# Kernel tuning notes

Measured on AMD Instinct MI355X. Metric: run time of the kernel, lower is better.

The kernel has to match this reference:

```python
import jax, jax.numpy as jnp
import numpy as np

# SuperposedExpert: K parallel TT-factorized FFN paths + holographic routing.
# d_model=1024 factorized as [32,32]; d_ff=4096 as [64,64]; tt_ranks=[1,16,1] (r0/r2 squeezed).
K, D_MODEL, D_FF, RANK = 4, 1024, 4096, 16
IN1, IN2 = 32, 32          # factorize_for_tt(d_model)
F1, F2 = 64, 64            # factorize_for_tt(d_ff)
TEMP = 1.0                 # routing_temperature


def setup_inputs() -> dict:
    key = jax.random.key(0)
    ks = jax.random.split(key, 8)
    s = 0.05
    tokens = jax.random.normal(ks[0], (2048, D_MODEL), dtype=jnp.float32)
    # TT cores for ffn1: d_model -> d_ff  (input_dims [32,32], output_dims [64,64])
    ffn1_core1 = jax.random.normal(ks[1], (K, IN1, F1, RANK), dtype=jnp.float32) * s
    ffn1_core2 = jax.random.normal(ks[2], (K, RANK, IN2, F2), dtype=jnp.float32) * s
    # TT cores for ffn2: d_ff -> d_model (input_dims [64,64], output_dims [32,32])
    ffn2_core1 = jax.random.normal(ks[3], (K, F1, IN1, RANK), dtype=jnp.float32) * s
    ffn2_core2 = jax.random.normal(ks[4], (K, RANK, F2, IN2), dtype=jnp.float32) * s
    # Holographic routing params (hd_dim == d_model -> identity HD projection)
    pb = jax.random.normal(ks[5], (K, D_MODEL), dtype=jnp.float32)
    path_bases = pb / jnp.linalg.norm(pb, axis=-1, keepdims=True)  # orthogonal-ish init
    path_weights = jax.random.normal(ks[6], (K, D_MODEL), dtype=jnp.float32) * s
    return {
        'tokens': tokens,
        'ffn1_core1': ffn1_core1, 'ffn1_core2': ffn1_core2,
        'ffn2_core1': ffn2_core1, 'ffn2_core2': ffn2_core2,
        'path_bases': path_bases, 'path_weights': path_weights,
    }


def reference(tokens, ffn1_core1, ffn1_core2, ffn2_core1, ffn2_core2,
              path_bases, path_weights):
    N = tokens.shape[0]
    # ---- K superposed TT-FFN paths ----
    x3 = tokens.reshape(N, IN1, IN2)  # [n, a, b]
    # TT matmul 1: y[x,y] = sum_{a,b,r} G1[a,x,r] G2[r,b,y] x[a,b]
    h = jnp.einsum('nab,kaxr,krby->knxy', x3, ffn1_core1, ffn1_core2)
    h = jax.nn.gelu(h.reshape(K, N, D_FF))  # quantum_activation stand-in
    h3 = h.reshape(K, N, F1, F2)
    y = jnp.einsum('knab,kaxr,krby->knxy', h3, ffn2_core1, ffn2_core2)
    y = y.reshape(K, N, D_MODEL)  # per-path outputs
    # ---- Holographic HD routing (hd_dim == d_model: identity projection) ----
    logits = jnp.einsum('nd,kd->nk', tokens, path_bases) / TEMP
    gates = jax.nn.softmax(logits, axis=-1)  # [n, k]
    # Collapse superposition: per-path elementwise HD modulation + gated sum
    out = jnp.einsum('knd,kd,nk->nd', y, 1.0 + path_weights, gates)
    return out
```

## Files before the change

kernel.cpp:

```cpp
#include <hip/hip_runtime.h>
#include <stdint.h>

#define GAS __attribute__((address_space(1)))
#define LAS __attribute__((address_space(3)))

typedef __attribute__((ext_vector_type(8))) short short8;
typedef __attribute__((ext_vector_type(16))) float f32x16;

static constexpr int N_TOK = 2048;
static constexpr int DM    = 1024;
static constexpr int DF    = 4096;
static constexpr int KP    = 4;

__device__ inline unsigned short f2bf(float f) {
  union { float f; uint32_t u; } v; v.f = f;
  uint32_t u = v.u;
  u += 0x7FFFu + ((u >> 16) & 1u);
  return (unsigned short)(u >> 16);
}

__device__ inline uint32_t pk_bf(float lo, float hi) {
  union { float f; uint32_t u; } a, b; a.f = lo; b.f = hi;
  uint32_t ul = a.u + 0x7FFFu + ((a.u >> 16) & 1u);
  uint32_t uh = b.u + 0x7FFFu + ((b.u >> 16) & 1u);
  return (ul >> 16) | (uh & 0xFFFF0000u);
}

__device__ inline float gelu_gate(float v, float g) {
  float t0 = v * v;
  float u  = v * __builtin_fmaf(t0, -0.10294456f, -2.3022539f);
  float e  = __builtin_amdgcn_exp2f(u);
  float r  = __builtin_amdgcn_rcpf(1.0f + e);
  return v * g * r;
}

__device__ inline void gld16(const void* g, void* l) {
  __builtin_amdgcn_global_load_lds((const GAS void*)g, (LAS void*)l, 16, 0, 0);
}

__global__ __launch_bounds__(256) void setup_kernel(
    const float* __restrict__ tokens, const float* __restrict__ pb,
    const float* __restrict__ c11, const float* __restrict__ c12,
    const float* __restrict__ c21, const float* __restrict__ c22,
    float* __restrict__ gates, unsigned short* __restrict__ xb,
    unsigned short* __restrict__ w1t, unsigned short* __restrict__ w2t) {
  __shared__ __align__(16) float sh[2048];
  const int blk = blockIdx.x;
  const int t = threadIdx.x;
  if (blk < 16384) {
    const int k = blk >> 12, f = blk & 4095;
    const int x = f >> 6, y = f & 63;
    float* s1 = sh;
    float* s2 = sh + 512;
    for (int i = t; i < 512; i += 256) {
      int a = i >> 4, r = i & 15;
      s1[i] = c11[(((size_t)(k * 32 + a)) * 64 + x) * 16 + r];
    }
    for (int i = t; i < 512; i += 256) {
      int r = i >> 5, b = i & 31;
      s2[i] = c12[(((size_t)(k * 16 + r)) * 32 + b) * 64 + y];
    }
    __syncthreads();
    unsigned short* wrow = w1t + ((size_t)k * DF + f) * DM;
    const int d0 = t * 4;
    const int a = d0 >> 5, b0 = d0 & 31;
    float4 s1q[4];
#pragma unroll
    for (int q = 0; q < 4; ++q) s1q[q] = *(const float4*)(s1 + a * 16 + q * 4);
    float4 acc = {0.f, 0.f, 0.f, 0.f};
#pragma unroll
    for (int r = 0; r < 16; ++r) {
      float cv = (r & 3) == 0 ? s1q[r >> 2].x : (r & 3) == 1 ? s1q[r >> 2].y
               : (r & 3) == 2 ? s1q[r >> 2].z : s1q[r >> 2].w;
      float4 bv = *(const float4*)(s2 + r * 32 + b0);
      acc.x = __builtin_fmaf(cv, bv.x, acc.x);
      acc.y = __builtin_fmaf(cv, bv.y, acc.y);
      acc.z = __builtin_fmaf(cv, bv.z, acc.z);
      acc.w = __builtin_fmaf(cv, bv.w, acc.w);
    }
    ushort4 o; o.x = f2bf(acc.x); o.y = f2bf(acc.y); o.z = f2bf(acc.z); o.w = f2bf(acc.w);
    *(ushort4*)(wrow + d0) = o;
  } else if (blk < 20480) {
    const int kd = blk - 16384;
    const int k = kd >> 10, d = kd & 1023;
    const int x = d >> 5, y = d & 31;
    float* s1 = sh;
    float* s2 = sh + 1024;
    for (int i = t; i < 1024; i += 256) {
      int a = i >> 4, r = i & 15;
      s1[i] = c21[(((size_t)(k * 64 + a)) * 32 + x) * 16 + r];
    }
    for (int i = t; i < 1024; i += 256) {
      int r = i >> 6, b = i & 63;
      s2[i] = c22[(((size_t)(k * 16 + r)) * 64 + b) * 32 + y];
    }
    __syncthreads();
    unsigned short* wrow = w2t + ((size_t)k * DM + d) * DF;
    const int a = t >> 2;
    const int b0 = (t * 16) & 63;
    float4 s1q[4];
#pragma unroll
    for (int q = 0; q < 4; ++q) s1q[q] = *(const float4*)(s1 + a * 16 + q * 4);
    float4 acc[4] = {{0.f,0.f,0.f,0.f},{0.f,0.f,0.f,0.f},{0.f,0.f,0.f,0.f},{0.f,0.f,0.f,0.f}};
#pragma unroll
    for (int r = 0; r < 16; ++r) {
      float cv = (r & 3) == 0 ? s1q[r >> 2].x : (r & 3) == 1 ? s1q[r >> 2].y
               : (r & 3) == 2 ? s1q[r >> 2].z : s1q[r >> 2].w;
#pragma unroll
      for (int c = 0; c < 4; ++c) {
        float4 bv = *(const float4*)(s2 + r * 64 + b0 + c * 4);
        acc[c].x = __builtin_fmaf(cv, bv.x, acc[c].x);
        acc[c].y = __builtin_fmaf(cv, bv.y, acc[c].y);
        acc[c].z = __builtin_fmaf(cv, bv.z, acc[c].z);
        acc[c].w = __builtin_fmaf(cv, bv.w, acc[c].w);
      }
    }
#pragma unroll
    for (int c = 0; c < 4; ++c) {
      ushort4 o; o.x = f2bf(acc[c].x); o.y = f2bf(acc[c].y);
      o.z = f2bf(acc[c].z); o.w = f2bf(acc[c].w);
      *(ushort4*)(wrow + t * 16 + c * 4) = o;
    }
  } else {
    const int wave = t >> 6, lane = t & 63;
    const int n = (blk - 20480) * 4 + wave;
    float s0 = 0.f, s1v = 0.f, s2v = 0.f, s3v = 0.f;
    const float4* tr = (const float4*)(tokens + (size_t)n * DM);
#pragma unroll
    for (int j = 0; j < 4; ++j) {
      int idx = j * 64 + lane;
      float4 tv = tr[idx];
      ushort4 b;
      b.x = f2bf(tv.x); b.y = f2bf(tv.y); b.z = f2bf(tv.z); b.w = f2bf(tv.w);
      *(ushort4*)(xb + (size_t)n * DM + idx * 4) = b;
      float4 q;
      q = ((const float4*)(pb + 0 * DM))[idx]; s0  += tv.x*q.x + tv.y*q.y + tv.z*q.z + tv.w*q.w;
      q = ((const float4*)(pb + 1 * DM))[idx]; s1v += tv.x*q.x + tv.y*q.y + tv.z*q.z + tv.w*q.w;
      q = ((const float4*)(pb + 2 * DM))[idx]; s2v += tv.x*q.x + tv.y*q.y + tv.z*q.z + tv.w*q.w;
      q = ((const float4*)(pb + 3 * DM))[idx]; s3v += tv.x*q.x + tv.y*q.y + tv.z*q.z + tv.w*q.w;
    }
#pragma unroll
    for (int off = 32; off > 0; off >>= 1) {
      s0  += __shfl_xor(s0, off);
      s1v += __shfl_xor(s1v, off);
      s2v += __shfl_xor(s2v, off);
      s3v += __shfl_xor(s3v, off);
    }
    if (lane == 0) {
      float m = fmaxf(fmaxf(s0, s1v), fmaxf(s2v, s3v));
      float e0 = __expf(s0 - m), e1 = __expf(s1v - m), e2 = __expf(s2v - m), e3 = __expf(s3v - m);
      float inv = 1.0f / (e0 + e1 + e2 + e3);
      float4 g; g.x = e0 * inv; g.y = e1 * inv; g.z = e2 * inv; g.w = e3 * inv;
      *(float4*)(gates + n * 4) = g;
    }
  }
}

__global__ __launch_bounds__(256) void gemm1(
    const unsigned short* __restrict__ xb, const unsigned short* __restrict__ w1t,
    const float* __restrict__ gates, unsigned short* __restrict__ hg) {
  __shared__ __align__(16) unsigned short As[128 * 64];
  __shared__ __align__(16) unsigned short Bs[128 * 64];
  const int t = threadIdx.x, lane = t & 63, wv = t >> 6;
  const int m0 = blockIdx.x * 128;
  const int f0 = blockIdx.y * 128;
  const int kp = blockIdx.z;
  const unsigned short* B = w1t + (size_t)kp * DF * DM;
  f32x16 acc[2][2] = {};
  const int srow = t >> 3;
  const int sbase = ((t & 7) ^ (srow & 7) ^ (srow >> 3)) * 8;
  const int wfrow = (wv >> 1) * 64, wtcol = (wv & 1) * 64;
  const int l31 = lane & 31, khalf = lane >> 5;
  const int rsw = (l31 & 7) ^ (l31 >> 3);
  char* AsB = (char*)As;
  char* BsB = (char*)Bs;
  for (int k0 = 0; k0 < DM; k0 += 64) {
#pragma unroll
    for (int i = 0; i < 4; ++i) {
      int row = i * 32 + srow;
      int sc = sbase ^ ((i & 1) * 32);
      gld16(xb + (size_t)(m0 + row) * DM + k0 + sc, AsB + i * 4096 + t * 16);
      gld16(B + (size_t)(f0 + row) * DM + k0 + sc, BsB + i * 4096 + t * 16);
    }
    __syncthreads();
#pragma unroll
    for (int s = 0; s < 4; ++s) {
      const int lc = s * 2 + khalf;
      short8 a[2], b[2];
#pragma unroll
      for (int mi = 0; mi < 2; ++mi) {
        const int pc = ((lc ^ rsw ^ (mi * 4)) & 7) * 8;
        a[mi] = *(const short8*)(Bs + (wfrow + mi * 32 + l31) * 64 + pc);
      }
#pragma unroll
      for (int ni = 0; ni < 2; ++ni) {
        const int pc = ((lc ^ rsw ^ (ni * 4)) & 7) * 8;
        b[ni] = *(const short8*)(As + (wtcol + ni * 32 + l31) * 64 + pc);
      }
#pragma unroll
      for (int mi = 0; mi < 2; ++mi)
#pragma unroll
        for (int ni = 0; ni < 2; ++ni)
          acc[mi][ni] = __builtin_amdgcn_mfma_f32_32x32x16_bf16(a[mi], b[ni], acc[mi][ni], 0, 0, 0);
    }
    __syncthreads();
  }
  unsigned short* H = hg + (size_t)kp * N_TOK * DF;
  const int rbase = 4 * khalf;
#pragma unroll
  for (int ni = 0; ni < 2; ++ni) {
    int n_g = m0 + wtcol + ni * 32 + l31;
    float g = gates[n_g * 4 + kp];
    unsigned short* hrow = H + (size_t)n_g * DF + f0;
#pragma unroll
    for (int mi = 0; mi < 2; ++mi) {
      int fbase = wfrow + mi * 32 + rbase;
#pragma unroll
      for (int gq = 0; gq < 4; ++gq) {
        float r0 = gelu_gate(acc[mi][ni][4 * gq + 0], g);
        float r1 = gelu_gate(acc[mi][ni][4 * gq + 1], g);
        float r2 = gelu_gate(acc[mi][ni][4 * gq + 2], g);
        float r3 = gelu_gate(acc[mi][ni][4 * gq + 3], g);
        uint2 p; p.x = pk_bf(r0, r1); p.y = pk_bf(r2, r3);
        *(uint2*)(hrow + fbase + 8 * gq) = p;
      }
    }
  }
}

__global__ __launch_bounds__(256) void gemm2(
    const unsigned short* __restrict__ hg, const unsigned short* __restrict__ w2t,
    const float* __restrict__ pw, float* __restrict__ part) {
  __shared__ __align__(16) unsigned short As[128 * 64];
  __shared__ __align__(16) unsigned short Bs[128 * 64];
  const int t = threadIdx.x, lane = t & 63, wv = t >> 6;
  const int m0 = blockIdx.x * 128;
  const int n0 = blockIdx.y * 128;
  const int kp = blockIdx.z;
  const unsigned short* A = hg + (size_t)kp * N_TOK * DF;
  const unsigned short* B = w2t + (size_t)kp * DM * DF;
  f32x16 acc[2][2] = {};
  const int srow = t >> 3;
  const int sbase = ((t & 7) ^ (srow & 7) ^ (srow >> 3)) * 8;
  const int wdrow = (wv >> 1) * 64, wtcol = (wv & 1) * 64;
  const int l31 = lane & 31, khalf = lane >> 5;
  const int rsw = (l31 & 7) ^ (l31 >> 3);
  char* AsB = (char*)As;
  char* BsB = (char*)Bs;
  for (int k0 = 0; k0 < DF; k0 += 64) {
#pragma unroll
    for (int i = 0; i < 4; ++i) {
      int row = i * 32 + srow;
      int sc = sbase ^ ((i & 1) * 32);
      gld16(A + (size_t)(m0 + row) * DF + k0 + sc, AsB + i * 4096 + t * 16);
      gld16(B + (size_t)(n0 + row) * DF + k0 + sc, BsB + i * 4096 + t * 16);
    }
    __syncthreads();
#pragma unroll
    for (int s = 0; s < 4; ++s) {
      const int lc = s * 2 + khalf;
      short8 a[2], b[2];
#pragma unroll
      for (int mi = 0; mi < 2; ++mi) {
        const int pc = ((lc ^ rsw ^ (mi * 4)) & 7) * 8;
        a[mi] = *(const short8*)(Bs + (wdrow + mi * 32 + l31) * 64 + pc);
      }
#pragma unroll
      for (int ni = 0; ni < 2; ++ni) {
        const int pc = ((lc ^ rsw ^ (ni * 4)) & 7) * 8;
        b[ni] = *(const short8*)(As + (wtcol + ni * 32 + l31) * 64 + pc);
      }
#pragma unroll
      for (int mi = 0; mi < 2; ++mi)
#pragma unroll
        for (int ni = 0; ni < 2; ++ni)
          acc[mi][ni] = __builtin_amdgcn_mfma_f32_32x32x16_bf16(a[mi], b[ni], acc[mi][ni], 0, 0, 0);
    }
    __syncthreads();
  }
  float* P = part + (size_t)kp * N_TOK * DM;
  const int rbase = 4 * khalf;
  float4 pwv[2][4];
#pragma unroll
  for (int mi = 0; mi < 2; ++mi)
#pragma unroll
    for (int gq = 0; gq < 4; ++gq) {
      float4 w = *(const float4*)(pw + kp * DM + n0 + wdrow + mi * 32 + rbase + 8 * gq);
      pwv[mi][gq].x = 1.0f + w.x; pwv[mi][gq].y = 1.0f + w.y;
      pwv[mi][gq].z = 1.0f + w.z; pwv[mi][gq].w = 1.0f + w.w;
    }
#pragma unroll
  for (int ni = 0; ni < 2; ++ni) {
    int tok = m0 + wtcol + ni * 32 + l31;
    float* prow = P + (size_t)tok * DM + n0;
#pragma unroll
    for (int mi = 0; mi < 2; ++mi) {
      int dbase = wdrow + mi * 32 + rbase;
#pragma unroll
      for (int gq = 0; gq < 4; ++gq) {
        float4 o;
        o.x = pwv[mi][gq].x * acc[mi][ni][4 * gq + 0];
        o.y = pwv[mi][gq].y * acc[mi][ni][4 * gq + 1];
        o.z = pwv[mi][gq].z * acc[mi][ni][4 * gq + 2];
        o.w = pwv[mi][gq].w * acc[mi][ni][4 * gq + 3];
        *(float4*)(prow + dbase + 8 * gq) = o;
      }
    }
  }
}

__global__ __launch_bounds__(256) void reduce_k(
    const float* __restrict__ part, float* __restrict__ out) {
  const size_t i = ((size_t)blockIdx.x * 256 + threadIdx.x) * 4;
  const size_t S = (size_t)N_TOK * DM;
  float4 a = *(const float4*)(part + i);
  float4 b = *(const float4*)(part + S + i);
  float4 c = *(const float4*)(part + 2 * S + i);
  float4 d = *(const float4*)(part + 3 * S + i);
  float4 r;
  r.x = a.x + b.x + c.x + d.x;
  r.y = a.y + b.y + c.y + d.y;
  r.z = a.z + b.z + c.z + d.z;
  r.w = a.w + b.w + c.w + d.w;
  *(float4*)(out + i) = r;
}

extern "C" void kernel_launch(void* const* d_in, const int* in_sizes, int n_in,
                              void* d_out, int out_size, void* d_ws, size_t ws_size,
                              hipStream_t stream) {
  const float* tokens = (const float*)d_in[0];
  const float* f1c1   = (const float*)d_in[1];
  const float* f1c2   = (const float*)d_in[2];
  const float* f2c1   = (const float*)d_in[3];
  const float* f2c2   = (const float*)d_in[4];
  const float* pb     = (const float*)d_in[5];
  const float* pw     = (const float*)d_in[6];
  float* out = (float*)d_out;

  char* ws = (char*)d_ws;
  unsigned short* xb  = (unsigned short*)(ws);
  unsigned short* w1t = (unsigned short*)(ws + (4ull  << 20));
  float*          part = (float*)(ws + (4ull << 20));
  unsigned short* w2t = (unsigned short*)(ws + (36ull << 20));
  unsigned short* hg  = (unsigned short*)(ws + (68ull << 20));
  float*          gates = (float*)(ws + (132ull << 20));

  hipLaunchKernelGGL(setup_kernel, dim3(20992), dim3(256), 0, stream,
                     tokens, pb, f1c1, f1c2, f2c1, f2c2, gates, xb, w1t, w2t);
  hipLaunchKernelGGL(gemm1, dim3(16, 32, KP), dim3(256), 0, stream, xb, w1t, gates, hg);
  hipLaunchKernelGGL(gemm2, dim3(16, 8, KP), dim3(256), 0, stream, hg, w2t, pw, part);
  hipLaunchKernelGGL(reduce_k, dim3(2048), dim3(256), 0, stream, part, out);
}
```

Before: 297.3 us.

## Batch TT weight expansion: each setup block builds 16 output rows with shared staging

The setup kernel that expands TT cores into dense bf16 weight matrices now has each block produce 16 output rows instead of one. It stages the second core transposed in padded shared memory with vectorized float4 loads, cutting the grid from 20992 to 1792 blocks. The intent is to remove the redundant, uncoalesced gather loads of core data that each single-row block repeated. The cost is much more shared memory per block (about 70KB) and a longer serial loop per thread, which lowers occupancy.

```diff
diff --git a/kernel.cpp b/kernel.cpp
--- a/kernel.cpp
+++ b/kernel.cpp
@@ -44,86 +44,97 @@
     const float* __restrict__ c21, const float* __restrict__ c22,
     float* __restrict__ gates, unsigned short* __restrict__ xb,
     unsigned short* __restrict__ w1t, unsigned short* __restrict__ w2t) {
-  __shared__ __align__(16) float sh[2048];
+  __shared__ __align__(16) float sh[17472];
   const int blk = blockIdx.x;
   const int t = threadIdx.x;
-  if (blk < 16384) {
-    const int k = blk >> 12, f = blk & 4095;
-    const int x = f >> 6, y = f & 63;
-    float* s1 = sh;
-    float* s2 = sh + 512;
-    for (int i = t; i < 512; i += 256) {
-      int a = i >> 4, r = i & 15;
-      s1[i] = c11[(((size_t)(k * 32 + a)) * 64 + x) * 16 + r];
-    }
-    for (int i = t; i < 512; i += 256) {
-      int r = i >> 5, b = i & 31;
-      s2[i] = c12[(((size_t)(k * 16 + r)) * 32 + b) * 64 + y];
-    }
-    __syncthreads();
-    unsigned short* wrow = w1t + ((size_t)k * DF + f) * DM;
-    const int d0 = t * 4;
-    const int a = d0 >> 5, b0 = d0 & 31;
+  if (blk < 1024) {
+    const int k = blk >> 8, x = (blk >> 2) & 63, y0 = (blk & 3) * 16;
+    float* s1  = sh;
+    float* s2T = sh + 512;
+    if (t < 128) {
+      int a = t >> 2, rq = (t & 3) * 4;
+      *(float4*)(s1 + a * 16 + rq) =
+          *(const float4*)(c11 + (((size_t)(k * 32 + a)) * 64 + x) * 16 + rq);
+    }
+#pragma unroll
+    for (int j = 0; j < 8; ++j) {
+      int i = t + j * 256;
+      int rb = i >> 2, yy0 = (i & 3) * 4;
+      float4 v = *(const float4*)(c12 + (size_t)(k * 16) * 2048 + (size_t)rb * 64 + y0 + yy0);
+      s2T[(yy0 + 0) * 524 + rb] = v.x;
+      s2T[(yy0 + 1) * 524 + rb] = v.y;
+      s2T[(yy0 + 2) * 524 + rb] = v.z;
+      s2T[(yy0 + 3) * 524 + rb] = v.w;
+    }
+    __syncthreads();
+    const int a = t >> 3, b0 = (t & 7) * 4;
     float4 s1q[4];
 #pragma unroll
     for (int q = 0; q < 4; ++q) s1q[q] = *(const float4*)(s1 + a * 16 + q * 4);
-    float4 acc = {0.f, 0.f, 0.f, 0.f};
-#pragma unroll
-    for (int r = 0; r < 16; ++r) {
-      float cv = (r & 3) == 0 ? s1q[r >> 2].x : (r & 3) == 1 ? s1q[r >> 2].y
-               : (r & 3) == 2 ? s1q[r >> 2].z : s1q[r >> 2].w;
-      float4 bv = *(const float4*)(s2 + r * 32 + b0);
-      acc.x = __builtin_fmaf(cv, bv.x, acc.x);
-      acc.y = __builtin_fmaf(cv, bv.y, acc.y);
-      acc.z = __builtin_fmaf(cv, bv.z, acc.z);
-      acc.w = __builtin_fmaf(cv, bv.w, acc.w);
-    }
-    ushort4 o; o.x = f2bf(acc.x); o.y = f2bf(acc.y); o.z = f2bf(acc.z); o.w = f2bf(acc.w);
-    *(ushort4*)(wrow + d0) = o;
-  } else if (blk < 20480) {
-    const int kd = blk - 16384;
-    const int k = kd >> 10, d = kd & 1023;
-    const int x = d >> 5, y = d & 31;
-    float* s1 = sh;
-    float* s2 = sh + 1024;
-    for (int i = t; i < 1024; i += 256) {
-      int a = i >> 4, r = i & 15;
-      s1[i] = c21[(((size_t)(k * 64 + a)) * 32 + x) * 16 + r];
-    }
-    for (int i = t; i < 1024; i += 256) {
-      int r = i >> 6, b = i & 63;
-      s2[i] = c22[(((size_t)(k * 16 + r)) * 64 + b) * 32 + y];
-    }
-    __syncthreads();
-    unsigned short* wrow = w2t + ((size_t)k * DM + d) * DF;
-    const int a = t >> 2;
-    const int b0 = (t * 16) & 63;
-    float4 s1q[4];
-#pragma unroll
-    for (int q = 0; q < 4; ++q) s1q[q] = *(const float4*)(s1 + a * 16 + q * 4);
-    float4 acc[4] = {{0.f,0.f,0.f,0.f},{0.f,0.f,0.f,0.f},{0.f,0.f,0.f,0.f},{0.f,0.f,0.f,0.f}};
-#pragma unroll
-    for (int r = 0; r < 16; ++r) {
-      float cv = (r & 3) == 0 ? s1q[r >> 2].x : (r & 3) == 1 ? s1q[r >> 2].y
-               : (r & 3) == 2 ? s1q[r >> 2].z : s1q[r >> 2].w;
-#pragma unroll
-      for (int c = 0; c < 4; ++c) {
-        float4 bv = *(const float4*)(s2 + r * 64 + b0 + c * 4);
-        acc[c].x = __builtin_fmaf(cv, bv.x, acc[c].x);
-        acc[c].y = __builtin_fmaf(cv, bv.y, acc[c].y);
-        acc[c].z = __builtin_fmaf(cv, bv.z, acc[c].z);
-        acc[c].w = __builtin_fmaf(cv, bv.w, acc[c].w);
-      }
-    }
-#pragma unroll
-    for (int c = 0; c < 4; ++c) {
-      ushort4 o; o.x = f2bf(acc[c].x); o.y = f2bf(acc[c].y);
-      o.z = f2bf(acc[c].z); o.w = f2bf(acc[c].w);
-      *(ushort4*)(wrow + t * 16 + c * 4) = o;
+    const float* a0s = (const float*)s1q;
+    for (int y = 0; y < 16; ++y) {
+      const float* s2y = s2T + y * 524;
+      float4 acc = {0.f, 0.f, 0.f, 0.f};
+#pragma unroll
+      for (int r = 0; r < 16; ++r) {
+        float cv = a0s[r];
+        float4 bv = *(const float4*)(s2y + r * 32 + b0);
+        acc.x = __builtin_fmaf(cv, bv.x, acc.x);
+        acc.y = __builtin_fmaf(cv, bv.y, acc.y);
+        acc.z = __builtin_fmaf(cv, bv.z, acc.z);
+        acc.w = __builtin_fmaf(cv, bv.w, acc.w);
+      }
+      ushort4 o; o.x = f2bf(acc.x); o.y = f2bf(acc.y); o.z = f2bf(acc.z); o.w = f2bf(acc.w);
+      *(ushort4*)(w1t + ((size_t)k * DF + x * 64 + y0 + y) * DM + t * 4) = o;
+    }
+  } else if (blk < 1280) {
+    const int bb = blk - 1024;
+    const int k = bb >> 6, x = (bb >> 1) & 31, y0 = (bb & 1) * 16;
+    float* s1  = sh;
+    float* s2T = sh + 1024;
+    {
+      int a = t >> 2, rq = (t & 3) * 4;
+      *(float4*)(s1 + a * 16 + rq) =
+          *(const float4*)(c21 + (((size_t)(k * 64 + a)) * 32 + x) * 16 + rq);
+    }
+#pragma unroll
+    for (int j = 0; j < 16; ++j) {
+      int i = t + j * 256;
+      int rb = i >> 2, yy0 = (i & 3) * 4;
+      float4 v = *(const float4*)(c22 + (size_t)(k * 16) * 2048 + (size_t)rb * 32 + y0 + yy0);
+      s2T[(yy0 + 0) * 1028 + rb] = v.x;
+      s2T[(yy0 + 1) * 1028 + rb] = v.y;
+      s2T[(yy0 + 2) * 1028 + rb] = v.z;
+      s2T[(yy0 + 3) * 1028 + rb] = v.w;
+    }
+    __syncthreads();
+    const int b0 = (t & 15) * 4;
+#pragma unroll
+    for (int jj = 0; jj < 4; ++jj) {
+      const int a = (t >> 4) + jj * 16;
+      float4 s1q[4];
+#pragma unroll
+      for (int q = 0; q < 4; ++q) s1q[q] = *(const float4*)(s1 + a * 16 + q * 4);
+      const float* a0s = (const float*)s1q;
+      for (int y = 0; y < 16; ++y) {
+        const float* s2y = s2T + y * 1028;
+        float4 acc = {0.f, 0.f, 0.f, 0.f};
+#pragma unroll
+        for (int r = 0; r < 16; ++r) {
+          float cv = a0s[r];
+          float4 bv = *(const float4*)(s2y + r * 64 + b0);
+          acc.x = __builtin_fmaf(cv, bv.x, acc.x);
+          acc.y = __builtin_fmaf(cv, bv.y, acc.y);
+          acc.z = __builtin_fmaf(cv, bv.z, acc.z);
+          acc.w = __builtin_fmaf(cv, bv.w, acc.w);
+        }
+        ushort4 o; o.x = f2bf(acc.x); o.y = f2bf(acc.y); o.z = f2bf(acc.z); o.w = f2bf(acc.w);
+        *(ushort4*)(w2t + ((size_t)k * DM + x * 32 + y0 + y) * DF + t * 4 + jj * 1024) = o;
+      }
     }
   } else {
     const int wave = t >> 6, lane = t & 63;
-    const int n = (blk - 20480) * 4 + wave;
+    const int n = (blk - 1280) * 4 + wave;
     float s0 = 0.f, s1v = 0.f, s2v = 0.f, s3v = 0.f;
     const float4* tr = (const float4*)(tokens + (size_t)n * DM);
 #pragma unroll
@@ -345,7 +356,7 @@
   unsigned short* hg  = (unsigned short*)(ws + (68ull << 20));
   float*          gates = (float*)(ws + (132ull << 20));
 
-  hipLaunchKernelGGL(setup_kernel, dim3(20992), dim3(256), 0, stream,
+  hipLaunchKernelGGL(setup_kernel, dim3(1792), dim3(256), 0, stream,
                      tokens, pb, f1c1, f1c2, f2c1, f2c2, gates, xb, w1t, w2t);
   hipLaunchKernelGGL(gemm1, dim3(16, 32, KP), dim3(256), 0, stream, xb, w1t, gates, hg);
   hipLaunchKernelGGL(gemm2, dim3(16, 8, KP), dim3(256), 0, stream, hg, w2t, pw, part);
```

Result: faster. 274.7 us, median of 2 (-7.6%).
